# Performance work log

Measured on AMD Instinct MI355X. Metric: run time of the kernel, lower is better.

The kernel has to match this reference:

```python
import jax, jax.numpy as jnp
import numpy as np

N, LQ, LK = 16, 1024, 1024
DQ = DK = DE = DP = 512          # head_dim_q, head_dim_k, embed_d, proj_d
DA = DE + DQ                      # attention output width (1024)
D2 = DE + 2 * DQ                  # transformer-block width after second concat (1536)
EPS = 1e-5


def layernorm(x, g, b):
    mu = jnp.mean(x, axis=-1, keepdims=True)
    var = jnp.var(x, axis=-1, keepdims=True)
    return (x - mu) * jax.lax.rsqrt(var + EPS) * g + b


def setup_inputs() -> dict:
    root = jax.random.key(0)
    ks = jax.random.split(root, 12)
    s = 0.02
    return {
        "value": jax.random.normal(ks[0], (N, LK, DK), jnp.float32),
        "key": jax.random.normal(ks[1], (N, LK, DK), jnp.float32),
        "query": jax.random.normal(ks[2], (N, LQ, DQ), jnp.float32),
        "Wk": jax.random.normal(ks[3], (DK, DP), jnp.float32) * s,
        "Wq": jax.random.normal(ks[4], (DQ, DP), jnp.float32) * s,
        "Wo": jax.random.normal(ks[5], (DK, DE), jnp.float32) * s,
        "bo": jnp.zeros((DE,), jnp.float32),
        "ga": jnp.ones((DA,), jnp.float32),
        "ba": jnp.zeros((DA,), jnp.float32),
        "g1": jnp.ones((D2,), jnp.float32),
        "b1": jnp.zeros((D2,), jnp.float32),
        "W1": jax.random.normal(ks[6], (D2, 2 * D2), jnp.float32) * s,
        "bf1": jnp.zeros((2 * D2,), jnp.float32),
        "W2": jax.random.normal(ks[7], (2 * D2, D2), jnp.float32) * s,
        "bf2": jnp.zeros((D2,), jnp.float32),
        "g2": jnp.ones((D2,), jnp.float32),
        "b2": jnp.zeros((D2,), jnp.float32),
    }


def reference(value, key, query, Wk, Wq, Wo, bo, ga, ba, g1, b1, W1, bf1, W2, bf2, g2, b2):
    # --- Attention (hand-rolled, full energy matrix as in the original) ---
    kp = jnp.einsum('nkd,dp->nkp', key, Wk)      # [n, LK, DP]
    qp = jnp.einsum('nqd,dp->nqp', query, Wq)    # [n, LQ, DP]
    energy = jnp.einsum('nqp,nkp->nqk', qp, kp)  # [n, LQ, LK]
    attn = jax.nn.softmax(energy / jnp.sqrt(jnp.float32(DP)), axis=2)
    out = jnp.einsum('nqk,nkh->nqh', attn, value)  # [n, LQ, DK]
    out = jnp.einsum('nqh,he->nqe', out, Wo) + bo  # [n, LQ, DE]
    combined = jnp.concatenate([out, query], axis=2)  # [n, LQ, DA]
    attn_out = layernorm(combined, ga, ba)
    # --- TransformerBlock tail ---
    x = jnp.concatenate([attn_out, query], axis=2)  # [n, LQ, D2]
    x = layernorm(x, g1, b1)
    h = jax.nn.relu(jnp.einsum('nqd,df->nqf', x, W1) + bf1)
    f = jnp.einsum('nqf,fd->nqd', h, W2) + bf2
    return layernorm(f, g2, b2)
```

## Files before the change

### kernel.cpp

```cpp
#include <hip/hip_runtime.h>


typedef __attribute__((ext_vector_type(8))) __bf16 bf16x8;
typedef __attribute__((ext_vector_type(4))) float f32x4;

#define DEV static __device__ __forceinline__

DEV unsigned short f2bf(float f) {
  union { float f; unsigned int u; } x; x.f = f;
  unsigned int u = x.u + 0x7fffu + ((x.u >> 16) & 1u);
  return (unsigned short)(u >> 16);
}

DEV void gll16(const void* g, void* l) {
  __builtin_amdgcn_global_load_lds(
      (const __attribute__((address_space(1))) void*)g,
      (__attribute__((address_space(3))) void*)l, 16, 0, 0);
}

template <typename CT, bool BIAS, bool RELU>
__global__ __launch_bounds__(256)
void gemm_bt(const unsigned short* __restrict__ A,
             const unsigned short* __restrict__ Bt,
             CT* __restrict__ C, const float* __restrict__ bias,
             int M, int N, int K,
             long long sA, long long sB, long long sC) {
  __shared__ __align__(16) unsigned short ldsA[128 * 32];
  __shared__ __align__(16) unsigned short ldsB[128 * 32];
  const int t = threadIdx.x;
  const int w = t >> 6, lane = t & 63;
  A  += (long long)blockIdx.z * sA;
  Bt += (long long)blockIdx.z * sB;
  C  += (long long)blockIdx.z * sC;
  const int rowBase = blockIdx.y * 128;
  const int colBase = blockIdx.x * 128;
  const int wm = w >> 1, wn = w & 1;

  const int c0 = t, c1 = t + 256;
  const int ra0 = c0 >> 2, ca0 = (c0 & 3) << 3;
  const int ra1 = c1 >> 2, ca1 = (c1 & 3) << 3;
  const unsigned short* gA0 = A + (long long)(rowBase + ra0) * K + ca0;
  const unsigned short* gA1 = A + (long long)(rowBase + ra1) * K + ca1;
  const unsigned short* gB0 = Bt + (long long)(colBase + ra0) * K + ca0;
  const unsigned short* gB1 = Bt + (long long)(colBase + ra1) * K + ca1;
  char* dA0 = (char*)ldsA + w * 1024;
  char* dA1 = (char*)ldsA + 4096 + w * 1024;
  char* dB0 = (char*)ldsB + w * 1024;
  char* dB1 = (char*)ldsB + 4096 + w * 1024;

  f32x4 acc[4][4];
#pragma unroll
  for (int m = 0; m < 4; ++m)
#pragma unroll
    for (int n = 0; n < 4; ++n) acc[m][n] = f32x4{0.f, 0.f, 0.f, 0.f};

  const unsigned short* pa = &ldsA[(wm * 64 + (lane & 15)) * 32 + ((lane >> 4) << 3)];
  const unsigned short* pb = &ldsB[(wn * 64 + (lane & 15)) * 32 + ((lane >> 4) << 3)];

  for (int k0 = 0; k0 < K; k0 += 32) {
    gll16(gA0 + k0, dA0);
    gll16(gA1 + k0, dA1);
    gll16(gB0 + k0, dB0);
    gll16(gB1 + k0, dB1);
    __syncthreads();
    bf16x8 av[4], bv[4];
#pragma unroll
    for (int m = 0; m < 4; ++m) av[m] = *(const bf16x8*)(pa + m * 512);
#pragma unroll
    for (int n = 0; n < 4; ++n) bv[n] = *(const bf16x8*)(pb + n * 512);
#pragma unroll
    for (int m = 0; m < 4; ++m)
#pragma unroll
      for (int n = 0; n < 4; ++n)
        acc[m][n] = __builtin_amdgcn_mfma_f32_16x16x32_bf16(av[m], bv[n], acc[m][n], 0, 0, 0);
    __syncthreads();
  }

  const int r0 = rowBase + wm * 64 + ((lane >> 4) << 2);
  const int cbase = colBase + wn * 64 + (lane & 15);
#pragma unroll
  for (int n = 0; n < 4; ++n) {
    const int col = cbase + n * 16;
    float bvv = 0.f;
    if constexpr (BIAS) bvv = bias[col];
#pragma unroll
    for (int m = 0; m < 4; ++m) {
#pragma unroll
      for (int r = 0; r < 4; ++r) {
        float v = acc[m][n][r] + bvv;
        if constexpr (RELU) v = v > 0.f ? v : 0.f;
        const long long idx = (long long)(r0 + m * 16 + r) * N + col;
        if constexpr (sizeof(CT) == 2) C[idx] = (CT)f2bf(v);
        else                           C[idx] = (CT)v;
      }
    }
  }
}

__global__ void transpose_cast_k(const float* __restrict__ src,
                                 unsigned short* __restrict__ dst,
                                 int R, int Ccols, long long sS, long long sD) {
  __shared__ float tile[32][33];
  src += (long long)blockIdx.z * sS;
  dst += (long long)blockIdx.z * sD;
  const int rb = blockIdx.y * 32, cb = blockIdx.x * 32;
  const int tx = threadIdx.x, ty = threadIdx.y;
#pragma unroll
  for (int k = 0; k < 4; ++k)
    tile[ty + k * 8][tx] = src[(long long)(rb + ty + k * 8) * Ccols + cb + tx];
  __syncthreads();
#pragma unroll
  for (int k = 0; k < 4; ++k)
    dst[(long long)(cb + ty + k * 8) * R + rb + tx] = f2bf(tile[tx][ty + k * 8]);
}

__global__ void cast_f32_bf16_k(const float* __restrict__ src,
                                unsigned short* __restrict__ dst, long long n4) {
  long long i = (long long)blockIdx.x * 256 + threadIdx.x;
  const long long stride = (long long)gridDim.x * 256;
  for (; i < n4; i += stride) {
    float4 v = ((const float4*)src)[i];
    ushort4 o;
    o.x = f2bf(v.x); o.y = f2bf(v.y); o.z = f2bf(v.z); o.w = f2bf(v.w);
    ((ushort4*)dst)[i] = o;
  }
}

__global__ __launch_bounds__(256)
void softmax_k(const float* __restrict__ E, unsigned short* __restrict__ P) {
  __shared__ float sm[8];
  const long long row = blockIdx.x;
  const int t = threadIdx.x, w = t >> 6, lane = t & 63;
  float4 v = ((const float4*)E)[row * 256 + t];
  const float scale = 0.044194173824159216f;
  v.x *= scale; v.y *= scale; v.z *= scale; v.w *= scale;
  float mx = fmaxf(fmaxf(v.x, v.y), fmaxf(v.z, v.w));
#pragma unroll
  for (int m = 1; m < 64; m <<= 1) mx = fmaxf(mx, __shfl_xor(mx, m));
  if (lane == 0) sm[w] = mx;
  __syncthreads();
  mx = fmaxf(fmaxf(sm[0], sm[1]), fmaxf(sm[2], sm[3]));
  float e0 = __expf(v.x - mx), e1 = __expf(v.y - mx);
  float e2 = __expf(v.z - mx), e3 = __expf(v.w - mx);
  float s = e0 + e1 + e2 + e3;
#pragma unroll
  for (int m = 1; m < 64; m <<= 1) s += __shfl_xor(s, m);
  if (lane == 0) sm[4 + w] = s;
  __syncthreads();
  s = sm[4] + sm[5] + sm[6] + sm[7];
  const float inv = 1.0f / s;
  ushort4 o;
  o.x = f2bf(e0 * inv); o.y = f2bf(e1 * inv);
  o.z = f2bf(e2 * inv); o.w = f2bf(e3 * inv);
  ((ushort4*)P)[row * 256 + t] = o;
}

DEV void breduce2(float& a, float& b, float* sm, int w, int lane) {
#pragma unroll
  for (int m = 1; m < 64; m <<= 1) { a += __shfl_xor(a, m); b += __shfl_xor(b, m); }
  if (lane == 0) { sm[w] = a; sm[4 + w] = b; }
  __syncthreads();
  a = sm[0] + sm[1] + sm[2] + sm[3];
  b = sm[4] + sm[5] + sm[6] + sm[7];
  __syncthreads();
}

__global__ __launch_bounds__(256)
void ln_concat_k(const float* __restrict__ out2, const float* __restrict__ query,
                 const float* __restrict__ ga, const float* __restrict__ ba,
                 const float* __restrict__ g1, const float* __restrict__ b1,
                 unsigned short* __restrict__ xln) {
  __shared__ float sm[8];
  const long long row = blockIdx.x;
  const int t = threadIdx.x, w = t >> 6, lane = t & 63;
  const float* o = out2 + row * 512;
  const float* q = query + row * 512;
  float c0 = o[t], c1 = o[t + 256], c2 = q[t], c3 = q[t + 256];
  float s = c0 + c1 + c2 + c3;
  float ss = c0 * c0 + c1 * c1 + c2 * c2 + c3 * c3;
  breduce2(s, ss, sm, w, lane);
  float mu = s * (1.0f / 1024.0f);
  float var = ss * (1.0f / 1024.0f) - mu * mu;
  float rs = rsqrtf(var + 1e-5f);
  float a0 = (c0 - mu) * rs * ga[t] + ba[t];
  float a1 = (c1 - mu) * rs * ga[t + 256] + ba[t + 256];
  float a2 = (c2 - mu) * rs * ga[t + 512] + ba[t + 512];
  float a3 = (c3 - mu) * rs * ga[t + 768] + ba[t + 768];
  float s2 = a0 + a1 + a2 + a3 + c2 + c3;
  float ss2 = a0*a0 + a1*a1 + a2*a2 + a3*a3 + c2*c2 + c3*c3;
  breduce2(s2, ss2, sm, w, lane);
  float mu2 = s2 * (1.0f / 1536.0f);
  float var2 = ss2 * (1.0f / 1536.0f) - mu2 * mu2;
  float rs2 = rsqrtf(var2 + 1e-5f);
  unsigned short* xr = xln + row * 1536;
  xr[t]        = f2bf((a0 - mu2) * rs2 * g1[t] + b1[t]);
  xr[t + 256]  = f2bf((a1 - mu2) * rs2 * g1[t + 256] + b1[t + 256]);
  xr[t + 512]  = f2bf((a2 - mu2) * rs2 * g1[t + 512] + b1[t + 512]);
  xr[t + 768]  = f2bf((a3 - mu2) * rs2 * g1[t + 768] + b1[t + 768]);
  xr[t + 1024] = f2bf((c2 - mu2) * rs2 * g1[t + 1024] + b1[t + 1024]);
  xr[t + 1280] = f2bf((c3 - mu2) * rs2 * g1[t + 1280] + b1[t + 1280]);
}

__global__ __launch_bounds__(256)
void ln_final_k(const float* __restrict__ f, const float* __restrict__ g2,
                const float* __restrict__ b2, float* __restrict__ out) {
  __shared__ float sm[8];
  const long long row = blockIdx.x;
  const int t = threadIdx.x, w = t >> 6, lane = t & 63;
  const float* fr = f + row * 1536;
  float v[6];
  float s = 0.f, ss = 0.f;
#pragma unroll
  for (int j = 0; j < 6; ++j) { v[j] = fr[t + j * 256]; s += v[j]; ss += v[j] * v[j]; }
  breduce2(s, ss, sm, w, lane);
  float mu = s * (1.0f / 1536.0f);
  float var = ss * (1.0f / 1536.0f) - mu * mu;
  float rs = rsqrtf(var + 1e-5f);
  float* orow = out + row * 1536;
#pragma unroll
  for (int j = 0; j < 6; ++j)
    orow[t + j * 256] = (v[j] - mu) * rs * g2[t + j * 256] + b2[t + j * 256];
}

extern "C" void kernel_launch(void* const* d_in, const int* in_sizes, int n_in,
                              void* d_out, int out_size, void* d_ws, size_t ws_size,
                              hipStream_t stream) {
  const float* value = (const float*)d_in[0];
  const float* key   = (const float*)d_in[1];
  const float* query = (const float*)d_in[2];
  const float* Wk  = (const float*)d_in[3];
  const float* Wq  = (const float*)d_in[4];
  const float* Wo  = (const float*)d_in[5];
  const float* bo  = (const float*)d_in[6];
  const float* ga  = (const float*)d_in[7];
  const float* ba  = (const float*)d_in[8];
  const float* g1  = (const float*)d_in[9];
  const float* b1  = (const float*)d_in[10];
  const float* W1  = (const float*)d_in[11];
  const float* bf1 = (const float*)d_in[12];
  const float* W2  = (const float*)d_in[13];
  const float* bf2 = (const float*)d_in[14];
  const float* g2  = (const float*)d_in[15];
  const float* b2  = (const float*)d_in[16];
  float* out = (float*)d_out;
  char* ws = (char*)d_ws;

  const size_t oW1T = 0;
  const size_t oWkT = 9437184;
  const size_t oWqT = 9961472;
  const size_t oWoT = 10485760;
  const size_t oVT  = 11010048;
  const size_t oKeyB = 27787264;
  const size_t oQryB = 44564480;
  const size_t oKp   = 61341696;
  const size_t oQp   = 78118912;
  const size_t oE    = 100663296;
  const size_t oP    = oKeyB;
  const size_t oO    = oKp;
  const size_t oOut2 = oQp;
  const size_t oXln  = 27787264;
  const size_t oH    = 100663296;
  const size_t oW2T  = 201326592;
  const size_t oF    = 0;

  unsigned short* W1T = (unsigned short*)(ws + oW1T);
  unsigned short* WkT = (unsigned short*)(ws + oWkT);
  unsigned short* WqT = (unsigned short*)(ws + oWqT);
  unsigned short* WoT = (unsigned short*)(ws + oWoT);
  unsigned short* W2T = (unsigned short*)(ws + oW2T);
  unsigned short* VT  = (unsigned short*)(ws + oVT);
  unsigned short* keyB = (unsigned short*)(ws + oKeyB);
  unsigned short* qryB = (unsigned short*)(ws + oQryB);
  unsigned short* kp  = (unsigned short*)(ws + oKp);
  unsigned short* qp  = (unsigned short*)(ws + oQp);
  float*          E   = (float*)(ws + oE);
  unsigned short* P   = (unsigned short*)(ws + oP);
  unsigned short* O   = (unsigned short*)(ws + oO);
  float*          out2 = (float*)(ws + oOut2);
  unsigned short* xln = (unsigned short*)(ws + oXln);
  unsigned short* h   = (unsigned short*)(ws + oH);
  float*          f   = (float*)(ws + oF);

  const dim3 tb(32, 8);
  transpose_cast_k<<<dim3(16, 16, 1), tb, 0, stream>>>(Wk, WkT, 512, 512, 0, 0);
  transpose_cast_k<<<dim3(16, 16, 1), tb, 0, stream>>>(Wq, WqT, 512, 512, 0, 0);
  transpose_cast_k<<<dim3(16, 16, 1), tb, 0, stream>>>(Wo, WoT, 512, 512, 0, 0);
  transpose_cast_k<<<dim3(96, 48, 1), tb, 0, stream>>>(W1, W1T, 1536, 3072, 0, 0);
  transpose_cast_k<<<dim3(48, 96, 1), tb, 0, stream>>>(W2, W2T, 3072, 1536, 0, 0);
  transpose_cast_k<<<dim3(16, 32, 16), tb, 0, stream>>>(value, VT, 1024, 512, 524288, 524288);
  cast_f32_bf16_k<<<2048, 256, 0, stream>>>(key,   keyB, 2097152);
  cast_f32_bf16_k<<<2048, 256, 0, stream>>>(query, qryB, 2097152);
  gemm_bt<unsigned short, false, false><<<dim3(4, 128, 1), 256, 0, stream>>>(
      keyB, WkT, kp, nullptr, 16384, 512, 512, 0, 0, 0);
  gemm_bt<unsigned short, false, false><<<dim3(4, 128, 1), 256, 0, stream>>>(
      qryB, WqT, qp, nullptr, 16384, 512, 512, 0, 0, 0);
  gemm_bt<float, false, false><<<dim3(8, 8, 16), 256, 0, stream>>>(
      qp, kp, E, nullptr, 1024, 1024, 512, 524288, 524288, 1048576);
  softmax_k<<<16384, 256, 0, stream>>>(E, P);
  gemm_bt<unsigned short, false, false><<<dim3(4, 8, 16), 256, 0, stream>>>(
      P, VT, O, nullptr, 1024, 512, 1024, 1048576, 524288, 524288);
  gemm_bt<float, true, false><<<dim3(4, 128, 1), 256, 0, stream>>>(
      O, WoT, out2, bo, 16384, 512, 512, 0, 0, 0);
  ln_concat_k<<<16384, 256, 0, stream>>>(out2, query, ga, ba, g1, b1, xln);
  gemm_bt<unsigned short, true, true><<<dim3(24, 128, 1), 256, 0, stream>>>(
      xln, W1T, h, bf1, 16384, 3072, 1536, 0, 0, 0);
  gemm_bt<float, true, false><<<dim3(12, 128, 1), 256, 0, stream>>>(
      h, W2T, f, bf2, 16384, 1536, 3072, 0, 0, 0);
  ln_final_k<<<16384, 256, 0, stream>>>(f, g2, b2, out);
}
```

Before: 864.2 us.

## Replace GEMM with 256x256-tile, 4-stage pipelined, swizzled kernel

Replaces the 128x128 single-buffered GEMM with a 256x256-tile, 512-thread kernel. It uses a 4-slot LDS ring with 3-deep global_load_lds prefetch and explicit vmcnt waits. LDS reads use an XOR swizzle, MFMA phases are split with setprio, and the 1D grid is remapped for XCD locality. The aim is to hide global load latency and raise data reuse per tile. In exchange it needs 128 KB of LDS, and small GEMMs launch only 128 blocks, which may underfill the GPU.

```diff
diff --git a/kernel.cpp b/kernel.cpp
--- a/kernel.cpp
+++ b/kernel.cpp
@@ -18,73 +18,129 @@
       (__attribute__((address_space(3))) void*)l, 16, 0, 0);
 }
 
+#define MFMA16(a, b, c) (c) = __builtin_amdgcn_mfma_f32_16x16x32_bf16((a), (b), (c), 0, 0, 0)
+
 template <typename CT, bool BIAS, bool RELU>
-__global__ __launch_bounds__(256)
-void gemm_bt(const unsigned short* __restrict__ A,
+__global__ __launch_bounds__(512, 2)
+void gemm256(const unsigned short* __restrict__ A,
              const unsigned short* __restrict__ Bt,
              CT* __restrict__ C, const float* __restrict__ bias,
-             int M, int N, int K,
+             int M, int N, int K, int nbx, int nby,
              long long sA, long long sB, long long sC) {
-  __shared__ __align__(16) unsigned short ldsA[128 * 32];
-  __shared__ __align__(16) unsigned short ldsB[128 * 32];
-  const int t = threadIdx.x;
-  const int w = t >> 6, lane = t & 63;
-  A  += (long long)blockIdx.z * sA;
-  Bt += (long long)blockIdx.z * sB;
-  C  += (long long)blockIdx.z * sC;
-  const int rowBase = blockIdx.y * 128;
-  const int colBase = blockIdx.x * 128;
-  const int wm = w >> 1, wn = w & 1;
-
-  const int c0 = t, c1 = t + 256;
-  const int ra0 = c0 >> 2, ca0 = (c0 & 3) << 3;
-  const int ra1 = c1 >> 2, ca1 = (c1 & 3) << 3;
-  const unsigned short* gA0 = A + (long long)(rowBase + ra0) * K + ca0;
-  const unsigned short* gA1 = A + (long long)(rowBase + ra1) * K + ca1;
-  const unsigned short* gB0 = Bt + (long long)(colBase + ra0) * K + ca0;
-  const unsigned short* gB1 = Bt + (long long)(colBase + ra1) * K + ca1;
-  char* dA0 = (char*)ldsA + w * 1024;
-  char* dA1 = (char*)ldsA + 4096 + w * 1024;
-  char* dB0 = (char*)ldsB + w * 1024;
-  char* dB1 = (char*)ldsB + 4096 + w * 1024;
-
-  f32x4 acc[4][4];
-#pragma unroll
-  for (int m = 0; m < 4; ++m)
+  __shared__ __align__(16) unsigned short lds[65536];
+
+  const int cpx = gridDim.x >> 3;
+  const int id = blockIdx.x;
+  const int swz = (id & 7) * cpx + (id >> 3);
+  const int nxy = nbx * nby;
+  const int bz = swz / nxy;
+  const int rxy = swz - bz * nxy;
+  const int by = rxy / nbx;
+  const int bx = rxy - by * nbx;
+
+  A  += (long long)bz * sA;
+  Bt += (long long)bz * sB;
+  C  += (long long)bz * sC;
+  const int rowBase = by * 256, colBase = bx * 256;
+
+  const int tid = threadIdx.x;
+  const int w = tid >> 6, lane = tid & 63;
+  const int wm = w >> 2, wn = w & 3;
+
+  const int lr = lane >> 2;
+  const int sc = (((lane & 3) ^ ((lane >> 3) & 3)) << 3);
+  const long long Kll = K;
+  const unsigned short* gA0 = A  + (long long)(rowBase + w * 16 + lr) * Kll + sc;
+  const unsigned short* gA1 = gA0 + 128 * Kll;
+  const unsigned short* gB0 = Bt + (long long)(colBase + w * 16 + lr) * Kll + sc;
+  const unsigned short* gB1 = gB0 + 128 * Kll;
+  char* const Lb = (char*)lds;
+  const int dA0 = w * 1024, dA1 = (w + 8) * 1024;
+
+  const int sig = (lane >> 4) ^ ((lane >> 1) & 3);
+  const int aoff = (wm * 128 + (lane & 15)) * 32 + sig * 8;
+  const int boff = (wn * 64 + (lane & 15)) * 32 + sig * 8;
+
+  f32x4 acc[8][4];
+#pragma unroll
+  for (int m = 0; m < 8; ++m)
 #pragma unroll
     for (int n = 0; n < 4; ++n) acc[m][n] = f32x4{0.f, 0.f, 0.f, 0.f};
 
-  const unsigned short* pa = &ldsA[(wm * 64 + (lane & 15)) * 32 + ((lane >> 4) << 3)];
-  const unsigned short* pb = &ldsB[(wn * 64 + (lane & 15)) * 32 + ((lane >> 4) << 3)];
-
-  for (int k0 = 0; k0 < K; k0 += 32) {
-    gll16(gA0 + k0, dA0);
-    gll16(gA1 + k0, dA1);
-    gll16(gB0 + k0, dB0);
-    gll16(gB1 + k0, dB1);
-    __syncthreads();
-    bf16x8 av[4], bv[4];
-#pragma unroll
-    for (int m = 0; m < 4; ++m) av[m] = *(const bf16x8*)(pa + m * 512);
-#pragma unroll
-    for (int n = 0; n < 4; ++n) bv[n] = *(const bf16x8*)(pb + n * 512);
-#pragma unroll
-    for (int m = 0; m < 4; ++m)
-#pragma unroll
-      for (int n = 0; n < 4; ++n)
-        acc[m][n] = __builtin_amdgcn_mfma_f32_16x16x32_bf16(av[m], bv[n], acc[m][n], 0, 0, 0);
-    __syncthreads();
+  const int NT = K >> 5;
+  const int npro = NT < 3 ? NT : 3;
+  for (int p = 0; p < npro; ++p) {
+    gll16(gA0 + (long long)p * 32, Lb + (p << 15) + dA0);
+    gll16(gA1 + (long long)p * 32, Lb + (p << 15) + dA1);
+    gll16(gB0 + (long long)p * 32, Lb + (p << 15) + 16384 + dA0);
+    gll16(gB1 + (long long)p * 32, Lb + (p << 15) + 16384 + dA1);
   }
-
-  const int r0 = rowBase + wm * 64 + ((lane >> 4) << 2);
-  const int cbase = colBase + wn * 64 + (lane & 15);
+  if (NT >= 3) asm volatile("s_waitcnt vmcnt(8)" ::: "memory");
+  else         asm volatile("s_waitcnt vmcnt(0)" ::: "memory");
+  __builtin_amdgcn_sched_barrier(0);
+  __builtin_amdgcn_s_barrier();
+  __builtin_amdgcn_sched_barrier(0);
+
+  for (int t = 0; t < NT; ++t) {
+    const int slot = t & 3;
+    const unsigned short* sa = lds + slot * 16384;
+    const unsigned short* sb = sa + 8192;
+    bf16x8 av[8];
+#pragma unroll
+    for (int m = 0; m < 8; ++m)
+      av[m] = *(const bf16x8*)(sa + aoff + m * 512);
+    bf16x8 bv0 = *(const bf16x8*)(sb + boff);
+    bf16x8 bv1 = *(const bf16x8*)(sb + boff + 512);
+    if (t + 3 < NT) {
+      const int ss = (t + 3) & 3;
+      gll16(gA0 + (long long)(t + 3) * 32, Lb + (ss << 15) + dA0);
+      gll16(gA1 + (long long)(t + 3) * 32, Lb + (ss << 15) + dA1);
+    }
+    __builtin_amdgcn_sched_barrier(0);
+    __builtin_amdgcn_s_barrier();
+    __builtin_amdgcn_sched_barrier(0);
+    __builtin_amdgcn_s_setprio(1);
+#pragma unroll
+    for (int m = 0; m < 8; ++m) {
+      MFMA16(av[m], bv0, acc[m][0]);
+      MFMA16(av[m], bv1, acc[m][1]);
+    }
+    __builtin_amdgcn_s_setprio(0);
+    __builtin_amdgcn_sched_barrier(0);
+    __builtin_amdgcn_s_barrier();
+    bf16x8 bv2 = *(const bf16x8*)(sb + boff + 1024);
+    bf16x8 bv3 = *(const bf16x8*)(sb + boff + 1536);
+    if (t + 3 < NT) {
+      const int ss = (t + 3) & 3;
+      gll16(gB0 + (long long)(t + 3) * 32, Lb + (ss << 15) + 16384 + dA0);
+      gll16(gB1 + (long long)(t + 3) * 32, Lb + (ss << 15) + 16384 + dA1);
+    }
+    if (t + 3 < NT)      asm volatile("s_waitcnt vmcnt(8)" ::: "memory");
+    else if (t + 2 < NT) asm volatile("s_waitcnt vmcnt(4)" ::: "memory");
+    else if (t + 1 < NT) asm volatile("s_waitcnt vmcnt(0)" ::: "memory");
+    __builtin_amdgcn_sched_barrier(0);
+    __builtin_amdgcn_s_barrier();
+    __builtin_amdgcn_sched_barrier(0);
+    __builtin_amdgcn_s_setprio(1);
+#pragma unroll
+    for (int m = 0; m < 8; ++m) {
+      MFMA16(av[m], bv2, acc[m][2]);
+      MFMA16(av[m], bv3, acc[m][3]);
+    }
+    __builtin_amdgcn_s_setprio(0);
+    __builtin_amdgcn_sched_barrier(0);
+    __builtin_amdgcn_s_barrier();
+  }
+
+  const int r0 = rowBase + wm * 128 + ((lane >> 4) << 2);
+  const int cb = colBase + wn * 64 + (lane & 15);
 #pragma unroll
   for (int n = 0; n < 4; ++n) {
-    const int col = cbase + n * 16;
+    const int col = cb + n * 16;
     float bvv = 0.f;
     if constexpr (BIAS) bvv = bias[col];
 #pragma unroll
-    for (int m = 0; m < 4; ++m) {
+    for (int m = 0; m < 8; ++m) {
 #pragma unroll
       for (int r = 0; r < 4; ++r) {
         float v = acc[m][n][r] + bvv;
@@ -290,21 +346,22 @@
   transpose_cast_k<<<dim3(16, 32, 16), tb, 0, stream>>>(value, VT, 1024, 512, 524288, 524288);
   cast_f32_bf16_k<<<2048, 256, 0, stream>>>(key,   keyB, 2097152);
   cast_f32_bf16_k<<<2048, 256, 0, stream>>>(query, qryB, 2097152);
-  gemm_bt<unsigned short, false, false><<<dim3(4, 128, 1), 256, 0, stream>>>(
-      keyB, WkT, kp, nullptr, 16384, 512, 512, 0, 0, 0);
-  gemm_bt<unsigned short, false, false><<<dim3(4, 128, 1), 256, 0, stream>>>(
-      qryB, WqT, qp, nullptr, 16384, 512, 512, 0, 0, 0);
-  gemm_bt<float, false, false><<<dim3(8, 8, 16), 256, 0, stream>>>(
-      qp, kp, E, nullptr, 1024, 1024, 512, 524288, 524288, 1048576);
+
+  gemm256<unsigned short, false, false><<<128, 512, 0, stream>>>(
+      keyB, WkT, kp, nullptr, 16384, 512, 512, 2, 64, 0, 0, 0);
+  gemm256<unsigned short, false, false><<<128, 512, 0, stream>>>(
+      qryB, WqT, qp, nullptr, 16384, 512, 512, 2, 64, 0, 0, 0);
+  gemm256<float, false, false><<<256, 512, 0, stream>>>(
+      qp, kp, E, nullptr, 1024, 1024, 512, 4, 4, 524288, 524288, 1048576);
   softmax_k<<<16384, 256, 0, stream>>>(E, P);
-  gemm_bt<unsigned short, false, false><<<dim3(4, 8, 16), 256, 0, stream>>>(
-      P, VT, O, nullptr, 1024, 512, 1024, 1048576, 524288, 524288);
-  gemm_bt<float, true, false><<<dim3(4, 128, 1), 256, 0, stream>>>(
-      O, WoT, out2, bo, 16384, 512, 512, 0, 0, 0);
+  gemm256<unsigned short, false, false><<<128, 512, 0, stream>>>(
+      P, VT, O, nullptr, 1024, 512, 1024, 2, 4, 1048576, 524288, 524288);
+  gemm256<float, true, false><<<128, 512, 0, stream>>>(
+      O, WoT, out2, bo, 16384, 512, 512, 2, 64, 0, 0, 0);
   ln_concat_k<<<16384, 256, 0, stream>>>(out2, query, ga, ba, g1, b1, xln);
-  gemm_bt<unsigned short, true, true><<<dim3(24, 128, 1), 256, 0, stream>>>(
-      xln, W1T, h, bf1, 16384, 3072, 1536, 0, 0, 0);
-  gemm_bt<float, true, false><<<dim3(12, 128, 1), 256, 0, stream>>>(
-      h, W2T, f, bf2, 16384, 1536, 3072, 0, 0, 0);
+  gemm256<unsigned short, true, true><<<768, 512, 0, stream>>>(
+      xln, W1T, h, bf1, 16384, 3072, 1536, 12, 64, 0, 0, 0);
+  gemm256<float, true, false><<<384, 512, 0, stream>>>(
+      h, W2T, f, bf2, 16384, 1536, 3072, 6, 64, 0, 0, 0);
   ln_final_k<<<16384, 256, 0, stream>>>(f, g2, b2, out);
 }
```

New measurement: 771.2 us. 1.12x faster.
